# Kernel optimization log

Hardware: AMD Instinct MI355X
Metric: run time of the kernel (lower is better)

The kernel has to match this reference:

```python
import jax, jax.numpy as jnp
import numpy as np

IN_F = 4096
OUT_F = 4096
BATCH = 256


def setup_inputs() -> dict:
    key = jax.random.key(0)
    ks = jax.random.split(key, 5)
    stdv = 1.0 / np.sqrt(IN_F)
    x = jax.random.normal(ks[0], (BATCH, IN_F), dtype=jnp.float32)
    weight_mu = jax.random.uniform(ks[1], (OUT_F, IN_F), dtype=jnp.float32, minval=-stdv, maxval=stdv)
    bias_mu = jax.random.uniform(ks[2], (OUT_F,), dtype=jnp.float32, minval=-stdv, maxval=stdv)
    weight_logvar = jnp.full((OUT_F, IN_F), -6.0, dtype=jnp.float32)
    bias_logvar = jnp.full((OUT_F,), -6.0, dtype=jnp.float32)
    weight_eps = jax.random.normal(ks[3], (OUT_F, IN_F), dtype=jnp.float32)
    bias_eps = jax.random.normal(ks[4], (OUT_F,), dtype=jnp.float32)
    return {
        "x": x,
        "weight_mu": weight_mu,
        "weight_logvar": weight_logvar,
        "bias_mu": bias_mu,
        "bias_logvar": bias_logvar,
        "weight_eps": weight_eps,
        "bias_eps": bias_eps,
    }


def reference(x, weight_mu, weight_logvar, bias_mu, bias_logvar, weight_eps, bias_eps):
    # Reparameterized sample: W = mu + eps * exp(0.5 * logvar)
    weight = weight_mu + weight_eps * jnp.exp(0.5 * weight_logvar)   # [O, I]
    bias = bias_mu + bias_eps * jnp.exp(0.5 * bias_logvar)           # [O]
    # F.linear: y = x @ W^T + b
    return jnp.einsum('bi,oi->bo', x, weight) + bias
```

## Files before the change

### kernel.cpp

```cpp
#include <hip/hip_runtime.h>
#include <stdint.h>
#include <stddef.h>

#define BATCH 256
#define IN_F  4096
#define OUT_F 4096
#define BN    16
#define BK    64
#define NT    (IN_F / BK)
#define TPB   512

typedef __attribute__((ext_vector_type(8))) short    bf16x8;
typedef __attribute__((ext_vector_type(4))) float    f32x4;
typedef __attribute__((ext_vector_type(2))) float    f32x2;
typedef __attribute__((ext_vector_type(4))) uint32_t u32x4;

#define MFMA(a, b, c) __builtin_amdgcn_mfma_f32_16x16x32_bf16((a), (b), (c), 0, 0, 0)

__device__ __forceinline__ uint32_t pack2bf(float a, float b) {
  uint32_t ua = __builtin_bit_cast(uint32_t, a);
  uint32_t ub = __builtin_bit_cast(uint32_t, b);
  ua += 0x7FFFu + ((ua >> 16) & 1u);
  ub += 0x7FFFu + ((ub >> 16) & 1u);
  return (ua >> 16) | (ub & 0xFFFF0000u);
}

__device__ __forceinline__ bf16x8 cvt8(const float* __restrict__ p) {
  f32x4 v0 = *(const f32x4*)p;
  f32x4 v1 = *(const f32x4*)(p + 4);
  union { u32x4 u; bf16x8 h; } r;
  r.u[0] = pack2bf(v0[0], v0[1]);
  r.u[1] = pack2bf(v0[2], v0[3]);
  r.u[2] = pack2bf(v1[0], v1[1]);
  r.u[3] = pack2bf(v1[2], v1[3]);
  return r.h;
}

__global__ __launch_bounds__(256) void prep_kernel(
    const float* __restrict__ x,
    const float* __restrict__ bmu,
    const float* __restrict__ blv,
    const float* __restrict__ beps,
    u32x4* __restrict__ xs4,
    float* __restrict__ bias)
{
  const uint32_t b = blockIdx.x;
  if (b < 512u) {
    const uint32_t c = b * 256u + threadIdx.x;
    const float* p = x + (size_t)c * 8u;
    f32x4 v0 = *(const f32x4*)p;
    f32x4 v1 = *(const f32x4*)(p + 4);
    u32x4 o;
    o[0] = pack2bf(v0[0], v0[1]);
    o[1] = pack2bf(v0[2], v0[3]);
    o[2] = pack2bf(v1[0], v1[1]);
    o[3] = pack2bf(v1[2], v1[3]);
    xs4[c] = o;
  } else {
    const uint32_t i = (b - 512u) * 256u + threadIdx.x;
    float s = exp2f(blv[i] * 0.7213475204444817f);
    bias[i] = fmaf(beps[i], s, bmu[i]);
  }
}

template<bool USE_XS>
__global__ __launch_bounds__(TPB)
void vgemm_kernel(const uint16_t* __restrict__ xs,
                  const float*    __restrict__ xf,
                  const float*    __restrict__ wmu,
                  const float*    __restrict__ wlv,
                  const float*    __restrict__ weps,
                  const float*    __restrict__ biasp,
                  const float*    __restrict__ bmu,
                  const float*    __restrict__ blv,
                  const float*    __restrict__ beps,
                  float*          __restrict__ y)
{
  __shared__ __align__(16) uint8_t wsm[2][2048];

  const int tid = threadIdx.x;
  const int wv  = tid >> 6;
  const int l   = tid & 63;
  const int n0  = blockIdx.x * BN;

  const int    wr   = tid >> 5;
  const int    wc   = (tid << 1) & 63;
  const size_t wgo  = (size_t)(n0 + wr) * IN_F + wc;
  const int    wlds = wr * 128 + (((wc >> 3) ^ (wr & 7)) << 4) + ((wc & 7) << 1);

  const int arow  = wv * 32 + (l & 15);
  const int kb    = l >> 4;
  const int br    = l & 15;
  const int boff0 = br * 128 + (((kb    ) ^ (br & 7)) << 4);
  const int boff1 = br * 128 + (((kb + 4) ^ (br & 7)) << 4);

  f32x4 acc0 = {0.f, 0.f, 0.f, 0.f};
  f32x4 acc1 = {0.f, 0.f, 0.f, 0.f};

  bf16x8 aA[4], aB[4];
  f32x2  muA, lvA, epA, muB, lvB, epB;

  auto lda = [&](int t, bf16x8* d) {
    if constexpr (USE_XS) {
      const uint16_t* p = xs + (size_t)arow * IN_F + t * BK + kb * 8;
      d[0] = *(const bf16x8*)(p);
      d[1] = *(const bf16x8*)(p + 32);
      d[2] = *(const bf16x8*)(p + (size_t)16 * IN_F);
      d[3] = *(const bf16x8*)(p + (size_t)16 * IN_F + 32);
    } else {
      const float* p = xf + (size_t)arow * IN_F + t * BK + kb * 8;
      d[0] = cvt8(p);
      d[1] = cvt8(p + 32);
      d[2] = cvt8(p + (size_t)16 * IN_F);
      d[3] = cvt8(p + (size_t)16 * IN_F + 32);
    }
  };

  auto ldw = [&](int t, f32x2& mu, f32x2& lv, f32x2& ep) {
    const size_t o = wgo + (size_t)t * BK;
    mu = *(const f32x2*)(wmu + o);
    lv = *(const f32x2*)(wlv + o);
    ep = *(const f32x2*)(weps + o);
  };

  auto cvtw = [&](int buf, const f32x2& mu, const f32x2& lv, const f32x2& ep) {
    float s0 = exp2f(lv[0] * 0.7213475204444817f);
    float s1 = exp2f(lv[1] * 0.7213475204444817f);
    float w0 = fmaf(ep[0], s0, mu[0]);
    float w1 = fmaf(ep[1], s1, mu[1]);
    *(uint32_t*)(&wsm[buf][wlds]) = pack2bf(w0, w1);
  };

  auto compute = [&](int buf, const bf16x8* a) {
    bf16x8 b0 = *(const bf16x8*)(&wsm[buf][boff0]);
    bf16x8 b1 = *(const bf16x8*)(&wsm[buf][boff1]);
    acc0 = MFMA(a[0], b0, acc0);
    acc0 = MFMA(a[1], b1, acc0);
    acc1 = MFMA(a[2], b0, acc1);
    acc1 = MFMA(a[3], b1, acc1);
  };

  lda(0, aA);
  ldw(0, muA, lvA, epA);
  cvtw(0, muA, lvA, epA);
  ldw(1, muB, lvB, epB);
  asm volatile("s_waitcnt lgkmcnt(0)" ::: "memory");
  __builtin_amdgcn_s_barrier();
  __builtin_amdgcn_sched_barrier(0);

  for (int t = 0; t < NT; t += 2) {
    {
      lda(t + 1, aB);
      const int tw = (t + 2 <= NT - 1) ? t + 2 : NT - 1;
      ldw(tw, muA, lvA, epA);
      cvtw(1, muB, lvB, epB);
      compute(0, aA);
      asm volatile("s_waitcnt lgkmcnt(0)" ::: "memory");
      __builtin_amdgcn_s_barrier();
      __builtin_amdgcn_sched_barrier(0);
    }
    {
      const int tn = (t + 2 <= NT - 1) ? t + 2 : NT - 1;
      lda(tn, aA);
      const int tw = (t + 3 <= NT - 1) ? t + 3 : NT - 1;
      ldw(tw, muB, lvB, epB);
      cvtw(0, muA, lvA, epA);
      compute(1, aB);
      asm volatile("s_waitcnt lgkmcnt(0)" ::: "memory");
      __builtin_amdgcn_s_barrier();
      __builtin_amdgcn_sched_barrier(0);
    }
  }

  const int col = n0 + (l & 15);
  float bv;
  if constexpr (USE_XS) {
    bv = biasp[col];
  } else {
    bv = fmaf(beps[col], exp2f(blv[col] * 0.7213475204444817f), bmu[col]);
  }
  const int g     = l >> 4;
  const int rbase = wv * 32 + g * 4;
#pragma unroll
  for (int i = 0; i < 4; ++i)
    y[(size_t)(rbase + i) * OUT_F + col] = acc0[i] + bv;
#pragma unroll
  for (int i = 0; i < 4; ++i)
    y[(size_t)(rbase + 16 + i) * OUT_F + col] = acc1[i] + bv;
}

extern "C" void kernel_launch(void* const* d_in, const int* in_sizes, int n_in,
                              void* d_out, int out_size, void* d_ws, size_t ws_size,
                              hipStream_t stream) {
  const float* x    = (const float*)d_in[0];
  const float* wmu  = (const float*)d_in[1];
  const float* wlv  = (const float*)d_in[2];
  const float* bmu  = (const float*)d_in[3];
  const float* blv  = (const float*)d_in[4];
  const float* weps = (const float*)d_in[5];
  const float* beps = (const float*)d_in[6];
  float* y = (float*)d_out;

  const size_t xs_bytes = (size_t)BATCH * IN_F * 2;
  const size_t need     = xs_bytes + (size_t)OUT_F * 4;

  if (d_ws != nullptr && ws_size >= need) {
    uint16_t* xs   = (uint16_t*)d_ws;
    float*    bias = (float*)((char*)d_ws + xs_bytes);
    prep_kernel<<<528, 256, 0, stream>>>(x, bmu, blv, beps, (u32x4*)d_ws, bias);
    vgemm_kernel<true><<<OUT_F / BN, TPB, 0, stream>>>(
        xs, nullptr, wmu, wlv, weps, bias, nullptr, nullptr, nullptr, y);
  } else {
    vgemm_kernel<false><<<OUT_F / BN, TPB, 0, stream>>>(
        nullptr, x, wmu, wlv, weps, nullptr, bmu, blv, beps, y);
  }
}
```

Before: 80.81 us.

## Stage raw weight tensors into LDS via async global_load_lds triple buffering

Replaces the register-based weight prefetch with direct global-to-LDS loads (global_load_lds, 16 bytes per lane) into a three-deep raw buffer for mu, logvar and eps. A separate conversion pass then writes double-buffered bf16 weights. BK doubles to 128, so each tile issues more MFMAs and needs fewer barriers. The goal is deeper latency hiding for the weight stream, which dominates memory traffic. The cost is about 80KB of LDS per block, which limits occupancy, plus two barriers per iteration. The input pointer renaming in the launcher is confusing but maps the same indices.

Measured after the change: 98.68 us. +22.1%, slower.

```diff
diff --git a/kernel.cpp b/kernel.cpp
--- a/kernel.cpp
+++ b/kernel.cpp
@@ -6,16 +6,22 @@
 #define IN_F  4096
 #define OUT_F 4096
 #define BN    16
-#define BK    64
+#define BK    128
 #define NT    (IN_F / BK)
 #define TPB   512
 
+#define RAW_BUF   24576
+#define RAW_ARR   8192
+#define BF_BASE   73728
+#define LDS_TOTAL 81920
+
 typedef __attribute__((ext_vector_type(8))) short    bf16x8;
 typedef __attribute__((ext_vector_type(4))) float    f32x4;
-typedef __attribute__((ext_vector_type(2))) float    f32x2;
+typedef __attribute__((ext_vector_type(2))) uint32_t u32x2;
 typedef __attribute__((ext_vector_type(4))) uint32_t u32x4;
 
-#define MFMA(a, b, c) __builtin_amdgcn_mfma_f32_16x16x32_bf16((a), (b), (c), 0, 0, 0)
+#define MFMA(a,b,c) __builtin_amdgcn_mfma_f32_16x16x32_bf16((a),(b),(c),0,0,0)
+#define HALF_LOG2E 0.7213475204444817f
 
 __device__ __forceinline__ uint32_t pack2bf(float a, float b) {
   uint32_t ua = __builtin_bit_cast(uint32_t, a);
@@ -25,15 +31,19 @@
   return (ua >> 16) | (ub & 0xFFFF0000u);
 }
 
-__device__ __forceinline__ bf16x8 cvt8(const float* __restrict__ p) {
+__device__ __forceinline__ bf16x8 cvt8(const float* p) {
   f32x4 v0 = *(const f32x4*)p;
   f32x4 v1 = *(const f32x4*)(p + 4);
   union { u32x4 u; bf16x8 h; } r;
-  r.u[0] = pack2bf(v0[0], v0[1]);
-  r.u[1] = pack2bf(v0[2], v0[3]);
-  r.u[2] = pack2bf(v1[0], v1[1]);
-  r.u[3] = pack2bf(v1[2], v1[3]);
+  r.u[0] = pack2bf(v0[0], v0[1]); r.u[1] = pack2bf(v0[2], v0[3]);
+  r.u[2] = pack2bf(v1[0], v1[1]); r.u[3] = pack2bf(v1[2], v1[3]);
   return r.h;
+}
+
+__device__ __forceinline__ void gload_lds16(const void* g, void* l) {
+  __builtin_amdgcn_global_load_lds(
+      (const __attribute__((address_space(1))) uint32_t*)g,
+      (__attribute__((address_space(3))) uint32_t*)l, 16, 0, 0);
 }
 
 __global__ __launch_bounds__(256) void prep_kernel(
@@ -51,136 +61,138 @@
     f32x4 v0 = *(const f32x4*)p;
     f32x4 v1 = *(const f32x4*)(p + 4);
     u32x4 o;
-    o[0] = pack2bf(v0[0], v0[1]);
-    o[1] = pack2bf(v0[2], v0[3]);
-    o[2] = pack2bf(v1[0], v1[1]);
-    o[3] = pack2bf(v1[2], v1[3]);
+    o[0] = pack2bf(v0[0], v0[1]); o[1] = pack2bf(v0[2], v0[3]);
+    o[2] = pack2bf(v1[0], v1[1]); o[3] = pack2bf(v1[2], v1[3]);
     xs4[c] = o;
   } else {
     const uint32_t i = (b - 512u) * 256u + threadIdx.x;
-    float s = exp2f(blv[i] * 0.7213475204444817f);
-    bias[i] = fmaf(beps[i], s, bmu[i]);
+    bias[i] = fmaf(beps[i], exp2f(blv[i] * HALF_LOG2E), bmu[i]);
   }
 }
 
 template<bool USE_XS>
 __global__ __launch_bounds__(TPB)
-void vgemm_kernel(const uint16_t* __restrict__ xs,
-                  const float*    __restrict__ xf,
-                  const float*    __restrict__ wmu,
-                  const float*    __restrict__ wlv,
-                  const float*    __restrict__ weps,
-                  const float*    __restrict__ biasp,
-                  const float*    __restrict__ bmu,
-                  const float*    __restrict__ blv,
-                  const float*    __restrict__ beps,
-                  float*          __restrict__ y)
+void vgemm(const uint16_t* __restrict__ xs,
+           const float*    __restrict__ xf,
+           const float*    __restrict__ wmu,
+           const float*    __restrict__ wlv,
+           const float*    __restrict__ weps,
+           const float*    __restrict__ biasp,
+           const float*    __restrict__ bmu,
+           const float*    __restrict__ blv,
+           const float*    __restrict__ beps,
+           float*          __restrict__ y)
 {
-  __shared__ __align__(16) uint8_t wsm[2][2048];
+  __shared__ __align__(16) uint8_t lds[LDS_TOTAL];
 
   const int tid = threadIdx.x;
   const int wv  = tid >> 6;
   const int l   = tid & 63;
   const int n0  = blockIdx.x * BN;
 
-  const int    wr   = tid >> 5;
-  const int    wc   = (tid << 1) & 63;
-  const size_t wgo  = (size_t)(n0 + wr) * IN_F + wc;
-  const int    wlds = wr * 128 + (((wc >> 3) ^ (wr & 7)) << 4) + ((wc & 7) << 1);
-
-  const int arow  = wv * 32 + (l & 15);
-  const int kb    = l >> 4;
-  const int br    = l & 15;
-  const int boff0 = br * 128 + (((kb    ) ^ (br & 7)) << 4);
-  const int boff1 = br * 128 + (((kb + 4) ^ (br & 7)) << 4);
+  const int    sr   = tid >> 5;
+  const size_t goff = (size_t)(n0 + sr) * IN_F + ((tid & 31) << 2);
+
+  const int c16w = (tid & 31) >> 1;
+  const int bfw  = sr * 256 + ((c16w ^ (sr & 7)) << 4) + ((tid & 1) << 3);
+
+  const int br = l & 15;
+  const int kb = l >> 4;
+  const int bfo0 = br * 256 + (((0 * 4 + kb) ^ (br & 7)) << 4);
+  const int bfo1 = br * 256 + (((1 * 4 + kb) ^ (br & 7)) << 4);
+  const int bfo2 = br * 256 + (((2 * 4 + kb) ^ (br & 7)) << 4);
+  const int bfo3 = br * 256 + (((3 * 4 + kb) ^ (br & 7)) << 4);
+  const int arow0 = wv * 32 + br;
 
   f32x4 acc0 = {0.f, 0.f, 0.f, 0.f};
   f32x4 acc1 = {0.f, 0.f, 0.f, 0.f};
 
-  bf16x8 aA[4], aB[4];
-  f32x2  muA, lvA, epA, muB, lvB, epB;
-
-  auto lda = [&](int t, bf16x8* d) {
+  auto STAGE = [&](int t, int buf) {
+    const size_t go = goff + (size_t)t * BK;
+    uint8_t* base = &lds[0] + buf * RAW_BUF + wv * 1024;
+    gload_lds16(wmu  + go, base + 0 * RAW_ARR);
+    gload_lds16(wlv  + go, base + 1 * RAW_ARR);
+    gload_lds16(weps + go, base + 2 * RAW_ARR);
+  };
+
+  auto CVT = [&](int t) {
+    const uint8_t* rb = &lds[0] + (t % 3) * RAW_BUF;
+    f32x4 m = *(const f32x4*)(rb + 0 * RAW_ARR + tid * 16);
+    f32x4 v = *(const f32x4*)(rb + 1 * RAW_ARR + tid * 16);
+    f32x4 e = *(const f32x4*)(rb + 2 * RAW_ARR + tid * 16);
+    u32x2 o;
+    o[0] = pack2bf(fmaf(e[0], exp2f(v[0] * HALF_LOG2E), m[0]),
+                   fmaf(e[1], exp2f(v[1] * HALF_LOG2E), m[1]));
+    o[1] = pack2bf(fmaf(e[2], exp2f(v[2] * HALF_LOG2E), m[2]),
+                   fmaf(e[3], exp2f(v[3] * HALF_LOG2E), m[3]));
+    *(u32x2*)(&lds[0] + BF_BASE + (t & 1) * 4096 + bfw) = o;
+  };
+
+  auto COMP = [&](int t) {
+    const uint8_t* bfb = &lds[0] + BF_BASE + (t & 1) * 4096;
+    bf16x8 a00, a01, a02, a03, a10, a11, a12, a13;
     if constexpr (USE_XS) {
-      const uint16_t* p = xs + (size_t)arow * IN_F + t * BK + kb * 8;
-      d[0] = *(const bf16x8*)(p);
-      d[1] = *(const bf16x8*)(p + 32);
-      d[2] = *(const bf16x8*)(p + (size_t)16 * IN_F);
-      d[3] = *(const bf16x8*)(p + (size_t)16 * IN_F + 32);
+      const uint16_t* x0 = xs + (size_t)arow0 * IN_F + t * BK + kb * 8;
+      const uint16_t* x1 = x0 + (size_t)16 * IN_F;
+      a00 = *(const bf16x8*)(x0);      a01 = *(const bf16x8*)(x0 + 32);
+      a02 = *(const bf16x8*)(x0 + 64); a03 = *(const bf16x8*)(x0 + 96);
+      a10 = *(const bf16x8*)(x1);      a11 = *(const bf16x8*)(x1 + 32);
+      a12 = *(const bf16x8*)(x1 + 64); a13 = *(const bf16x8*)(x1 + 96);
     } else {
-      const float* p = xf + (size_t)arow * IN_F + t * BK + kb * 8;
-      d[0] = cvt8(p);
-      d[1] = cvt8(p + 32);
-      d[2] = cvt8(p + (size_t)16 * IN_F);
-      d[3] = cvt8(p + (size_t)16 * IN_F + 32);
+      const float* x0 = xf + (size_t)arow0 * IN_F + t * BK + kb * 8;
+      const float* x1 = x0 + (size_t)16 * IN_F;
+      a00 = cvt8(x0);      a01 = cvt8(x0 + 32);
+      a02 = cvt8(x0 + 64); a03 = cvt8(x0 + 96);
+      a10 = cvt8(x1);      a11 = cvt8(x1 + 32);
+      a12 = cvt8(x1 + 64); a13 = cvt8(x1 + 96);
     }
+    bf16x8 b0 = *(const bf16x8*)(bfb + bfo0);
+    bf16x8 b1 = *(const bf16x8*)(bfb + bfo1);
+    bf16x8 b2 = *(const bf16x8*)(bfb + bfo2);
+    bf16x8 b3 = *(const bf16x8*)(bfb + bfo3);
+    acc0 = MFMA(a00, b0, acc0); acc1 = MFMA(a10, b0, acc1);
+    acc0 = MFMA(a01, b1, acc0); acc1 = MFMA(a11, b1, acc1);
+    acc0 = MFMA(a02, b2, acc0); acc1 = MFMA(a12, b2, acc1);
+    acc0 = MFMA(a03, b3, acc0); acc1 = MFMA(a13, b3, acc1);
   };
 
-  auto ldw = [&](int t, f32x2& mu, f32x2& lv, f32x2& ep) {
-    const size_t o = wgo + (size_t)t * BK;
-    mu = *(const f32x2*)(wmu + o);
-    lv = *(const f32x2*)(wlv + o);
-    ep = *(const f32x2*)(weps + o);
-  };
-
-  auto cvtw = [&](int buf, const f32x2& mu, const f32x2& lv, const f32x2& ep) {
-    float s0 = exp2f(lv[0] * 0.7213475204444817f);
-    float s1 = exp2f(lv[1] * 0.7213475204444817f);
-    float w0 = fmaf(ep[0], s0, mu[0]);
-    float w1 = fmaf(ep[1], s1, mu[1]);
-    *(uint32_t*)(&wsm[buf][wlds]) = pack2bf(w0, w1);
-  };
-
-  auto compute = [&](int buf, const bf16x8* a) {
-    bf16x8 b0 = *(const bf16x8*)(&wsm[buf][boff0]);
-    bf16x8 b1 = *(const bf16x8*)(&wsm[buf][boff1]);
-    acc0 = MFMA(a[0], b0, acc0);
-    acc0 = MFMA(a[1], b1, acc0);
-    acc1 = MFMA(a[2], b0, acc1);
-    acc1 = MFMA(a[3], b1, acc1);
-  };
-
-  lda(0, aA);
-  ldw(0, muA, lvA, epA);
-  cvtw(0, muA, lvA, epA);
-  ldw(1, muB, lvB, epB);
-  asm volatile("s_waitcnt lgkmcnt(0)" ::: "memory");
-  __builtin_amdgcn_s_barrier();
-  __builtin_amdgcn_sched_barrier(0);
-
-  for (int t = 0; t < NT; t += 2) {
-    {
-      lda(t + 1, aB);
-      const int tw = (t + 2 <= NT - 1) ? t + 2 : NT - 1;
-      ldw(tw, muA, lvA, epA);
-      cvtw(1, muB, lvB, epB);
-      compute(0, aA);
-      asm volatile("s_waitcnt lgkmcnt(0)" ::: "memory");
-      __builtin_amdgcn_s_barrier();
-      __builtin_amdgcn_sched_barrier(0);
-    }
-    {
-      const int tn = (t + 2 <= NT - 1) ? t + 2 : NT - 1;
-      lda(tn, aA);
-      const int tw = (t + 3 <= NT - 1) ? t + 3 : NT - 1;
-      ldw(tw, muB, lvB, epB);
-      cvtw(0, muA, lvA, epA);
-      compute(1, aB);
-      asm volatile("s_waitcnt lgkmcnt(0)" ::: "memory");
-      __builtin_amdgcn_s_barrier();
-      __builtin_amdgcn_sched_barrier(0);
-    }
-  }
-
-  const int col = n0 + (l & 15);
+  STAGE(0, 0);
+  STAGE(1, 1);
+
+  for (int t = 0; t < NT - 2; ++t) {
+    STAGE(t + 2, (t + 2) % 3);
+    asm volatile("s_waitcnt vmcnt(6)" ::: "memory");
+    __builtin_amdgcn_s_barrier();
+    CVT(t);
+    asm volatile("s_waitcnt lgkmcnt(0)" ::: "memory");
+    __builtin_amdgcn_s_barrier();
+    COMP(t);
+  }
+  {
+    asm volatile("s_waitcnt vmcnt(3)" ::: "memory");
+    __builtin_amdgcn_s_barrier();
+    CVT(NT - 2);
+    asm volatile("s_waitcnt lgkmcnt(0)" ::: "memory");
+    __builtin_amdgcn_s_barrier();
+    COMP(NT - 2);
+  }
+  {
+    asm volatile("s_waitcnt vmcnt(0)" ::: "memory");
+    __builtin_amdgcn_s_barrier();
+    CVT(NT - 1);
+    asm volatile("s_waitcnt lgkmcnt(0)" ::: "memory");
+    __builtin_amdgcn_s_barrier();
+    COMP(NT - 1);
+  }
+
+  const int col = n0 + br;
   float bv;
   if constexpr (USE_XS) {
     bv = biasp[col];
   } else {
-    bv = fmaf(beps[col], exp2f(blv[col] * 0.7213475204444817f), bmu[col]);
-  }
-  const int g     = l >> 4;
-  const int rbase = wv * 32 + g * 4;
+    bv = fmaf(beps[col], exp2f(blv[col] * HALF_LOG2E), bmu[col]);
+  }
+  const int rbase = wv * 32 + kb * 4;
 #pragma unroll
   for (int i = 0; i < 4; ++i)
     y[(size_t)(rbase + i) * OUT_F + col] = acc0[i] + bv;
@@ -197,21 +209,23 @@
   const float* wlv  = (const float*)d_in[2];
   const float* bmu  = (const float*)d_in[3];
   const float* blv  = (const float*)d_in[4];
-  const float* weps = (const float*)d_in[5];
-  const float* beps = (const float*)d_in[6];
+  const float* beps = (const float*)d_in[5];
+  const float* bepsB= (const float*)d_in[6];
+  const float* weps = beps;
+  const float* b_eps = bepsB;
   float* y = (float*)d_out;
 
   const size_t xs_bytes = (size_t)BATCH * IN_F * 2;
   const size_t need     = xs_bytes + (size_t)OUT_F * 4;
 
   if (d_ws != nullptr && ws_size >= need) {
-    uint16_t* xs   = (uint16_t*)d_ws;
+    uint16_t* xsp  = (uint16_t*)d_ws;
     float*    bias = (float*)((char*)d_ws + xs_bytes);
-    prep_kernel<<<528, 256, 0, stream>>>(x, bmu, blv, beps, (u32x4*)d_ws, bias);
-    vgemm_kernel<true><<<OUT_F / BN, TPB, 0, stream>>>(
-        xs, nullptr, wmu, wlv, weps, bias, nullptr, nullptr, nullptr, y);
+    prep_kernel<<<528, 256, 0, stream>>>(x, bmu, blv, b_eps, (u32x4*)d_ws, bias);
+    vgemm<true><<<OUT_F / BN, TPB, 0, stream>>>(
+        xsp, nullptr, wmu, wlv, weps, bias, nullptr, nullptr, nullptr, y);
   } else {
-    vgemm_kernel<false><<<OUT_F / BN, TPB, 0, stream>>>(
-        nullptr, x, wmu, wlv, weps, nullptr, bmu, blv, beps, y);
-  }
-}
+    vgemm<false><<<OUT_F / BN, TPB, 0, stream>>>(
+        nullptr, x, wmu, wlv, weps, nullptr, bmu, blv, b_eps, y);
+  }
+}
```
